# Optimization experiments

Measured on AMD Instinct MI355X. Metric: run time of the kernel, lower is better.

## Reference

```python
import jax, jax.numpy as jnp
import numpy as np

EPS = 1e-5
NUM_HEADS = 32

def layer_norm(x, g, b):
    m = jnp.mean(x, axis=-1, keepdims=True)
    v = jnp.mean((x - m) ** 2, axis=-1, keepdims=True)
    return (x - m) * jax.lax.rsqrt(v + EPS) * g + b

def positional_encoding(S, E):
    pos = jnp.arange(S, dtype=jnp.float32)[:, None]
    div = jnp.exp(jnp.arange(0, E, 2, dtype=jnp.float32) * (-jnp.log(10000.0) / E))
    ang = pos * div  # [S, E/2]
    pe = jnp.zeros((S, E), jnp.float32)
    pe = pe.at[:, 0::2].set(jnp.sin(ang)).at[:, 1::2].set(jnp.cos(ang))
    return pe

def quantum_attention(x, phi_l):
    # QLayer circuit: RX(x_j + phi_j) per wire, CNOT ring, measure Z.
    # Heisenberg picture: <Z_i> = prod_{j<=i} cos(a_j) for i>=1,
    #                     <Z_0> = prod_{j>=1} cos(a_j), a_j = x_j + phi_j.
    B, S, E = x.shape
    dk = E // NUM_HEADS  # = 8 wires
    c = jnp.cos(x.reshape(B, S, NUM_HEADS, dk) + phi_l)  # per-wire <Z> factor
    pref = jnp.cumprod(c, axis=-1)                       # prod_{j<=i}
    out0 = jnp.prod(c[..., 1:], axis=-1)                 # wire 0
    q = jnp.concatenate([out0[..., None], pref[..., 1:]], axis=-1)
    q = q.reshape(B, S, E)
    scores = jax.nn.softmax(
        jnp.einsum('bse,bte->bst', q, q) / jnp.sqrt(jnp.float32(dk)), axis=-1)
    return jnp.einsum('bst,bte->bse', scores, q)

def quantum_ffn(x, theta_l, W1_l, b1_l, W2_l, b2_l):
    # QLayer: RX(x_i) then RY(theta_i) on |0>, product state => <Z_i>=cos(x_i)cos(theta_i)
    nq = theta_l.shape[0]  # 8; encoder only reads first nq features
    qm = jnp.cos(x[..., :nq]) * jnp.cos(theta_l)
    h = jax.nn.relu(qm @ W1_l + b1_l)
    return h @ W2_l + b2_l

def setup_inputs() -> dict:
    key = jax.random.key(0)
    ks = jax.random.split(key, 10)
    V, E, L, FF, NQ, NC = 32000, 256, 4, 1024, 8, 10
    B, S = 8, 2048
    return {
        'tokens': jax.random.randint(ks[0], (B, S), 0, V, dtype=jnp.int64)
            if jax.config.jax_enable_x64 else jax.random.randint(ks[0], (B, S), 0, V, dtype=jnp.int32),
        'emb': jax.random.normal(ks[1], (V, E), jnp.float32),
        'phi': jax.random.normal(ks[2], (L, NQ), jnp.float32),
        'theta': jax.random.normal(ks[3], (L, NQ), jnp.float32),
        'W1': jax.random.normal(ks[4], (L, NQ, FF), jnp.float32) * 0.1,
        'b1': jax.random.normal(ks[5], (L, FF), jnp.float32) * 0.1,
        'W2': jax.random.normal(ks[6], (L, FF, E), jnp.float32) * 0.05,
        'b2': jax.random.normal(ks[7], (L, E), jnp.float32) * 0.05,
        'g1': jnp.ones((L, E), jnp.float32),
        'beta1': jnp.zeros((L, E), jnp.float32),
        'g2': jnp.ones((L, E), jnp.float32),
        'beta2': jnp.zeros((L, E), jnp.float32),
        'Wc': jax.random.normal(ks[8], (E, NC), jnp.float32) * 0.05,
        'bc': jax.random.normal(ks[9], (NC,), jnp.float32) * 0.05,
    }

def reference(tokens, emb, phi, theta, W1, b1, W2, b2, g1, beta1, g2, beta2, Wc, bc):
    B, S = tokens.shape
    E = emb.shape[1]
    x = emb[tokens] + positional_encoding(S, E)
    for l in range(phi.shape[0]):  # fixed num_blocks loop
        a = quantum_attention(x, phi[l])
        x = layer_norm(x + a, g1[l], beta1[l])
        f = quantum_ffn(x, theta[l], W1[l], b1[l], W2[l], b2[l])
        x = layer_norm(x + f, g2[l], beta2[l])
    return jnp.mean(x, axis=1) @ Wc + bc
```

## Files before the change

kernel.cpp:

```cpp
#include <hip/hip_runtime.h>
#include <hip/hip_bf16.h>

#define B_ 8
#define S_ 2048
#define E_ 256
#define FF_ 1024
#define NQ_ 8
#define NC_ 10
#define BS_ (B_*S_)
#define NSPLIT 2
#define KVBLK 32

typedef __bf16 bf16x8 __attribute__((ext_vector_type(8)));
typedef __bf16 bf16x4 __attribute__((ext_vector_type(4)));
typedef float f32x4 __attribute__((ext_vector_type(4)));

#define MFMA16(a,b,c) __builtin_amdgcn_mfma_f32_16x16x32_bf16(a,b,c,0,0,0)

__global__ __launch_bounds__(256) void k_embed(const int* __restrict__ tokens,
                                               const float* __restrict__ emb,
                                               float* __restrict__ x) {
    int row = blockIdx.x;
    int e = threadIdx.x;
    int s = row & (S_ - 1);
    int tok = tokens[row];
    int i2 = e & ~1;
    float d = __expf((float)i2 * (-9.210340371976184f / 256.0f));
    float ang = (float)s * d;
    float pe = (e & 1) ? __cosf(ang) : __sinf(ang);
    x[(size_t)row * E_ + e] = emb[(size_t)tok * E_ + e] + pe;
}

__global__ __launch_bounds__(256) void k_qt(const float* __restrict__ x,
                                            const float* __restrict__ phi_l,
                                            __hip_bfloat16* __restrict__ qbf,
                                            __hip_bfloat16* __restrict__ qT) {
    __shared__ __align__(16) __bf16 tile[64][76];
    int t0 = blockIdx.x * 64, e0 = blockIdx.y * 64, b = blockIdx.z;
    int tid = threadIdx.x;
    float ph[8];
#pragma unroll
    for (int j = 0; j < 8; j++) ph[j] = phi_l[j];
#pragma unroll
    for (int k = 0; k < 2; k++) {
        int idx = k * 256 + tid;
        int r = idx >> 3, hh = idx & 7;
        const float* xp = x + ((size_t)b * S_ + t0 + r) * E_ + e0 + hh * 8;
        f32x4 x0 = *(const f32x4*)xp;
        f32x4 x1 = *(const f32x4*)(xp + 4);
        float c[8];
#pragma unroll
        for (int j = 0; j < 4; j++) {
            c[j]     = __cosf(x0[j] + ph[j]);
            c[4 + j] = __cosf(x1[j] + ph[4 + j]);
        }
        float q[8];
        float run = c[0];
#pragma unroll
        for (int i = 1; i < 8; i++) { run *= c[i]; q[i] = run; }
        float o0 = c[1];
#pragma unroll
        for (int i = 2; i < 8; i++) o0 *= c[i];
        q[0] = o0;
        bf16x8 v;
#pragma unroll
        for (int j = 0; j < 8; j++) v[j] = (__bf16)q[j];
        *(bf16x8*)(qbf + ((size_t)b * S_ + t0 + r) * E_ + e0 + hh * 8) = v;
        *(bf16x8*)&tile[r][hh * 8] = v;
    }
    __syncthreads();
#pragma unroll
    for (int k = 0; k < 2; k++) {
        int idx = k * 256 + tid;
        int el = idx >> 3, tc = idx & 7;
        bf16x8 v;
#pragma unroll
        for (int j = 0; j < 8; j++) v[j] = tile[tc * 8 + j][el];
        *(bf16x8*)(qT + ((size_t)b * E_ + e0 + el) * S_ + t0 + tc * 8) = v;
    }
}

__global__ __launch_bounds__(256, 2) void k_attn(const __hip_bfloat16* __restrict__ qbf,
                                                 const __hip_bfloat16* __restrict__ qT,
                                                 __bf16* __restrict__ pacc,
                                                 float* __restrict__ pl) {
    __shared__ __align__(16) __bf16 ktile[KVBLK * 256];
    __shared__ __align__(16) __bf16 vtile[2][256 * KVBLK];
    __shared__ __align__(16) __bf16 plds[2][32][36];
    __shared__ float redl[2][32][2];
    const float SCALE = 0.3535533905932738f;
    int bid  = blockIdx.x;
    int b    = bid & 7;
    int qt   = (bid >> 3) & 31;
    int z    = bid >> 8;
    int tid  = threadIdx.x;
    int wv   = tid >> 6;
    int lane = tid & 63;
    int r16  = lane & 15;
    int kg   = lane >> 4;
    int rg   = wv >> 1, eh = wv & 1;
    int qrow0 = qt * 64 + rg * 32;
    int ebase = eh * 128;

    bf16x8 aq[2][8];
#pragma unroll
    for (int qs = 0; qs < 2; qs++)
#pragma unroll
        for (int kk = 0; kk < 8; kk++)
            aq[qs][kk] = *(const bf16x8*)(qbf + ((size_t)b * S_ + qrow0 + qs * 16 + r16) * E_ + kk * 32 + kg * 8);

    f32x4 acc0[8], acc1[8];
#pragma unroll
    for (int cf = 0; cf < 8; cf++) { acc0[cf] = (f32x4){0.f,0.f,0.f,0.f}; acc1[cf] = (f32x4){0.f,0.f,0.f,0.f}; }
    float lrow0[4] = {0.f,0.f,0.f,0.f}, lrow1[4] = {0.f,0.f,0.f,0.f};

    constexpr int SPAN = S_ / NSPLIT;
    constexpr int NT = SPAN / KVBLK;
    int k0 = z * SPAN;

    auto issue_k = [&](int kb) {
#pragma unroll
        for (int c = 0; c < 4; c++) {
            int seg = wv * 4 + c;
            int r = seg * 2 + (lane >> 5);
            int ch = lane & 31;
            const __hip_bfloat16* src = qbf + ((size_t)b * S_ + kb + r) * E_ + ((ch ^ (r & 7)) * 8);
            __builtin_amdgcn_global_load_lds((const __attribute__((address_space(1))) void*)src,
                                             (__attribute__((address_space(3))) void*)(ktile + seg * 512),
                                             16, 0, 0);
        }
    };
    auto issue_v = [&](int kb, int buf) {
#pragma unroll
        for (int c = 0; c < 4; c++) {
            int seg = wv * 4 + c;
            int e = seg * 16 + (lane >> 2);
            int ch = lane & 3;
            const __hip_bfloat16* src = qT + ((size_t)b * E_ + e) * S_ + kb + ((ch ^ ((e >> 1) & 3)) * 8);
            __builtin_amdgcn_global_load_lds((const __attribute__((address_space(1))) void*)src,
                                             (__attribute__((address_space(3))) void*)(&vtile[buf][seg * 512]),
                                             16, 0, 0);
        }
    };

    issue_k(k0);
    issue_v(k0, 0);
    asm volatile("s_waitcnt vmcnt(0)" ::: "memory");
    __syncthreads();

    for (int kt = 0; kt < NT; kt++) {
        int vcur = kt & 1;
        f32x4 s0 = (f32x4){0.f,0.f,0.f,0.f}, s1 = (f32x4){0.f,0.f,0.f,0.f};
#pragma unroll
        for (int kk = 0; kk < 8; kk++) {
            bf16x8 bk = *(const bf16x8*)&ktile[(eh * 16 + r16) * 256 + (((kk * 4 + kg) ^ (r16 & 7)) * 8)];
            s0 = MFMA16(aq[0][kk], bk, s0);
            s1 = MFMA16(aq[1][kk], bk, s1);
        }
#pragma unroll
        for (int i = 0; i < 4; i++) {
            float p0 = __expf(fmaf(s0[i], SCALE, -44.0f));
            float p1 = __expf(fmaf(s1[i], SCALE, -44.0f));
            plds[rg][kg * 4 + i][eh * 16 + r16]      = (__bf16)p0;
            plds[rg][16 + kg * 4 + i][eh * 16 + r16] = (__bf16)p1;
            lrow0[i] += p0;
            lrow1[i] += p1;
        }
        __syncthreads();
        bool more = (kt + 1 < NT);
        if (more) {
            int kn = k0 + (kt + 1) * KVBLK;
            issue_k(kn);
            issue_v(kn, vcur ^ 1);
        }
        bf16x8 pa0 = *(const bf16x8*)&plds[rg][r16][kg * 8];
        bf16x8 pa1 = *(const bf16x8*)&plds[rg][16 + r16][kg * 8];
#pragma unroll
        for (int cf = 0; cf < 8; cf++) {
            int vrow = ebase + cf * 16 + r16;
            bf16x8 bv = *(const bf16x8*)&vtile[vcur][vrow * KVBLK + ((kg ^ ((vrow >> 1) & 3)) * 8)];
            acc0[cf] = MFMA16(pa0, bv, acc0[cf]);
            acc1[cf] = MFMA16(pa1, bv, acc1[cf]);
        }
        if (more) {
            asm volatile("s_waitcnt vmcnt(0)" ::: "memory");
            __syncthreads();
        }
    }

#pragma unroll
    for (int i = 0; i < 4; i++) {
#pragma unroll
        for (int m = 1; m <= 8; m <<= 1) {
            lrow0[i] += __shfl_xor(lrow0[i], m);
            lrow1[i] += __shfl_xor(lrow1[i], m);
        }
    }
    if (r16 == 0) {
#pragma unroll
        for (int i = 0; i < 4; i++) {
            redl[rg][kg * 4 + i][eh]      = lrow0[i];
            redl[rg][16 + kg * 4 + i][eh] = lrow1[i];
        }
    }
    __syncthreads();
    size_t prow0 = (size_t)z * BS_ + (size_t)b * S_ + qrow0;
    if (eh == 0 && r16 == 0) {
#pragma unroll
        for (int i = 0; i < 4; i++) {
            int q = kg * 4 + i;
            pl[prow0 + q]      = redl[rg][q][0] + redl[rg][q][1];
            pl[prow0 + 16 + q] = redl[rg][16 + q][0] + redl[rg][16 + q][1];
        }
    }
#pragma unroll
    for (int i = 0; i < 4; i++) {
#pragma unroll
        for (int cf = 0; cf < 8; cf++) {
            pacc[(prow0 + kg * 4 + i) * E_ + ebase + cf * 16 + r16]      = (__bf16)acc0[cf][i];
            pacc[(prow0 + 16 + kg * 4 + i) * E_ + ebase + cf * 16 + r16] = (__bf16)acc1[cf][i];
        }
    }
}

__global__ __launch_bounds__(256) void k_aln(const __bf16* __restrict__ pacc,
                                             const float* __restrict__ pl,
                                             float* __restrict__ x,
                                             const float* __restrict__ g,
                                             const float* __restrict__ bb) {
    int wv = threadIdx.x >> 6, lane = threadIdx.x & 63;
    size_t row = (size_t)blockIdx.x * 4 + wv;
    float inv = 1.0f / (pl[row] + pl[BS_ + row]);
    bf16x4 a0 = ((const bf16x4*)(pacc + row * E_))[lane];
    bf16x4 a1 = ((const bf16x4*)(pacc + (size_t)BS_ * E_ + row * E_))[lane];
    f32x4 xv = ((const f32x4*)(x + row * E_))[lane];
    f32x4 v;
    float s = 0.f, sq = 0.f;
#pragma unroll
    for (int j = 0; j < 4; j++) {
        v[j] = xv[j] + ((float)a0[j] + (float)a1[j]) * inv;
        s += v[j]; sq += v[j] * v[j];
    }
#pragma unroll
    for (int m = 1; m <= 32; m <<= 1) { s += __shfl_xor(s, m); sq += __shfl_xor(sq, m); }
    float mean = s * (1.f / E_);
    float var = sq * (1.f / E_) - mean * mean;
    float rstd = rsqrtf(var + 1e-5f);
    f32x4 gv = ((const f32x4*)g)[lane];
    f32x4 bv = ((const f32x4*)bb)[lane];
    f32x4 o;
#pragma unroll
    for (int j = 0; j < 4; j++) o[j] = (v[j] - mean) * rstd * gv[j] + bv[j];
    ((f32x4*)(x + row * E_))[lane] = o;
}

__global__ __launch_bounds__(256) void k_w2t(const float* __restrict__ W2l,
                                             __hip_bfloat16* __restrict__ w2t) {
    __shared__ __align__(16) __bf16 tile[64][72];
    int k0 = blockIdx.x * 64, e0 = blockIdx.y * 64;
    int tid = threadIdx.x;
#pragma unroll
    for (int half = 0; half < 2; half++) {
        int r  = half * 32 + (tid >> 3);
        int c8 = (tid & 7) * 8;
        f32x4 v0 = *(const f32x4*)(W2l + (size_t)(k0 + r) * E_ + e0 + c8);
        f32x4 v1 = *(const f32x4*)(W2l + (size_t)(k0 + r) * E_ + e0 + c8 + 4);
#pragma unroll
        for (int j = 0; j < 4; j++) { tile[r][c8 + j] = (__bf16)v0[j]; tile[r][c8 + 4 + j] = (__bf16)v1[j]; }
    }
    __syncthreads();
#pragma unroll
    for (int half = 0; half < 2; half++) {
        int e  = half * 32 + (tid >> 3);
        int k8 = (tid & 7) * 8;
        bf16x8 v;
#pragma unroll
        for (int j = 0; j < 8; j++) v[j] = tile[k8 + j][e];
        *(bf16x8*)(w2t + (size_t)(e0 + e) * FF_ + k0 + k8) = v;
    }
}

__global__ __launch_bounds__(256) void k_ffn(const float* __restrict__ x,
                                             const float* __restrict__ theta_l,
                                             const float* __restrict__ W1l,
                                             const float* __restrict__ b1l,
                                             const __hip_bfloat16* __restrict__ w2t,
                                             const float* __restrict__ b2l,
                                             const float* __restrict__ g,
                                             const float* __restrict__ bb) {
    __shared__ __align__(16) __bf16 Bld[2][256 * 64];
    __shared__ __align__(16) __bf16 Ald[2][32 * 64];
    __shared__ float qmld[32][9];
    __shared__ float reds[32][4][2];
    int tid = threadIdx.x;
    int wv = tid >> 6, lane = tid & 63;
    int r16 = lane & 15, kg = lane >> 4;
    int rbase = blockIdx.x * 32;
    int ebQ = wv * 64;
    const int NT = FF_ / 64;

    {
        int r = tid >> 3, i = tid & 7;
        qmld[r][i] = __cosf(x[(size_t)(rbase + r) * E_ + i]) * __cosf(theta_l[i]);
    }

    f32x4 w[18];

    auto issue_B = [&](int kt, int buf) {
#pragma unroll
        for (int s = 0; s < 8; s++) {
            int seg = wv * 8 + s;
            int e = seg * 8 + (lane >> 3);
            int c = lane & 7;
            const __hip_bfloat16* src = w2t + (size_t)e * FF_ + kt * 64 + ((c ^ (e & 7)) * 8);
            __builtin_amdgcn_global_load_lds((const __attribute__((address_space(1))) void*)src,
                                             (__attribute__((address_space(3))) void*)(&Bld[buf][seg * 512]),
                                             16, 0, 0);
        }
    };
    auto load_W1 = [&](int kt) {
        int c = tid & 7;
        int k = kt * 64 + c * 8;
#pragma unroll
        for (int i = 0; i < 8; i++) {
            w[2 * i]     = *(const f32x4*)(W1l + (size_t)i * FF_ + k);
            w[2 * i + 1] = *(const f32x4*)(W1l + (size_t)i * FF_ + k + 4);
        }
        w[16] = *(const f32x4*)(b1l + k);
        w[17] = *(const f32x4*)(b1l + k + 4);
    };
    auto math_h = [&](int buf) {
        int r = tid >> 3, c = tid & 7;
        f32x4 h0 = w[16], h1 = w[17];
#pragma unroll
        for (int i = 0; i < 8; i++) {
            float qv = qmld[r][i];
#pragma unroll
            for (int j = 0; j < 4; j++) {
                h0[j] = fmaf(qv, w[2 * i][j], h0[j]);
                h1[j] = fmaf(qv, w[2 * i + 1][j], h1[j]);
            }
        }
        bf16x8 hv;
#pragma unroll
        for (int j = 0; j < 4; j++) {
            hv[j]     = (__bf16)fmaxf(h0[j], 0.f);
            hv[4 + j] = (__bf16)fmaxf(h1[j], 0.f);
        }
        *(bf16x8*)&Ald[buf][r * 64 + ((c ^ (r & 7)) * 8)] = hv;
    };

    issue_B(0, 0);
    load_W1(0);
    __syncthreads();
    math_h(0);
    __syncthreads();

    f32x4 acc[2][4];
#pragma unroll
    for (int qs = 0; qs < 2; qs++)
#pragma unroll
        for (int cf = 0; cf < 4; cf++) acc[qs][cf] = (f32x4){0.f, 0.f, 0.f, 0.f};

    for (int kt = 0; kt < NT; kt++) {
        int cur = kt & 1;
        bool more = (kt + 1 < NT);
        if (more) {
            issue_B(kt + 1, cur ^ 1);
            load_W1(kt + 1);
        }
        bf16x8 aq[2][2];
#pragma unroll
        for (int qs = 0; qs < 2; qs++)
#pragma unroll
            for (int kk = 0; kk < 2; kk++)
                aq[qs][kk] = *(const bf16x8*)&Ald[cur][(qs * 16 + r16) * 64 + (((kk * 4 + kg) ^ (r16 & 7)) * 8)];
#pragma unroll
        for (int cf = 0; cf < 4; cf++) {
            int e = ebQ + cf * 16 + r16;
#pragma unroll
            for (int kk = 0; kk < 2; kk++) {
                bf16x8 bv = *(const bf16x8*)&Bld[cur][e * 64 + (((kk * 4 + kg) ^ (e & 7)) * 8)];
                acc[0][cf] = MFMA16(aq[0][kk], bv, acc[0][cf]);
                acc[1][cf] = MFMA16(aq[1][kk], bv, acc[1][cf]);
            }
        }
        if (more) {
            math_h(cur ^ 1);
            __syncthreads();
        }
    }

    float sA[2][4] = {{0.f,0.f,0.f,0.f},{0.f,0.f,0.f,0.f}};
    float sQ[2][4] = {{0.f,0.f,0.f,0.f},{0.f,0.f,0.f,0.f}};
#pragma unroll
    for (int qs = 0; qs < 2; qs++)
#pragma unroll
        for (int cf = 0; cf < 4; cf++) {
            int e = ebQ + cf * 16 + r16;
            float b2v = b2l[e];
#pragma unroll
            for (int i = 0; i < 4; i++) {
                size_t orow = (size_t)rbase + qs * 16 + kg * 4 + i;
                float t = acc[qs][cf][i] + b2v + x[orow * E_ + e];
                acc[qs][cf][i] = t;
                sA[qs][i] += t; sQ[qs][i] += t * t;
            }
        }
#pragma unroll
    for (int qs = 0; qs < 2; qs++)
#pragma unroll
        for (int i = 0; i < 4; i++) {
#pragma unroll
            for (int m = 1; m <= 8; m <<= 1) {
                sA[qs][i] += __shfl_xor(sA[qs][i], m);
                sQ[qs][i] += __shfl_xor(sQ[qs][i], m);
            }
        }
    if (r16 == 0) {
#pragma unroll
        for (int qs = 0; qs < 2; qs++)
#pragma unroll
            for (int i = 0; i < 4; i++) {
                int row = qs * 16 + kg * 4 + i;
                reds[row][wv][0] = sA[qs][i];
                reds[row][wv][1] = sQ[qs][i];
            }
    }
    __syncthreads();
    float mean[2][4], rstd[2][4];
#pragma unroll
    for (int qs = 0; qs < 2; qs++)
#pragma unroll
        for (int i = 0; i < 4; i++) {
            int row = qs * 16 + kg * 4 + i;
            float S = reds[row][0][0] + reds[row][1][0] + reds[row][2][0] + reds[row][3][0];
            float Q = reds[row][0][1] + reds[row][1][1] + reds[row][2][1] + reds[row][3][1];
            mean[qs][i] = S * (1.f / E_);
            float var = Q * (1.f / E_) - mean[qs][i] * mean[qs][i];
            rstd[qs][i] = rsqrtf(var + 1e-5f);
        }
    float* xo = (float*)x;
#pragma unroll
    for (int qs = 0; qs < 2; qs++)
#pragma unroll
        for (int cf = 0; cf < 4; cf++) {
            int e = ebQ + cf * 16 + r16;
            float gv = g[e], bv = bb[e];
#pragma unroll
            for (int i = 0; i < 4; i++) {
                size_t orow = (size_t)rbase + qs * 16 + kg * 4 + i;
                xo[orow * E_ + e] = (acc[qs][cf][i] - mean[qs][i]) * rstd[qs][i] * gv + bv;
            }
        }
}

__global__ __launch_bounds__(256) void k_mean(const float* __restrict__ x, float* __restrict__ psum) {
    int c = blockIdx.x, b = blockIdx.y, e = threadIdx.x;
    float s = 0.f;
    size_t base = ((size_t)b * S_ + c * 128) * E_ + e;
    for (int r = 0; r < 128; r++) s += x[base + (size_t)r * E_];
    psum[(c * 8 + b) * E_ + e] = s;
}

__global__ __launch_bounds__(256) void k_mean2(const float* __restrict__ psum, float* __restrict__ xmean) {
    int idx = blockIdx.x * 256 + threadIdx.x;
    int b = idx >> 8, e = idx & 255;
    float s = 0.f;
    for (int c = 0; c < 16; c++) s += psum[(c * 8 + b) * E_ + e];
    xmean[idx] = s * (1.f / S_);
}

__global__ __launch_bounds__(128) void k_cls(const float* __restrict__ xmean,
                                             const float* __restrict__ Wc,
                                             const float* __restrict__ bc,
                                             float* __restrict__ outp) {
    int t = threadIdx.x;
    if (t >= B_ * NC_) return;
    int b = t / NC_, c = t % NC_;
    float s = bc[c];
    for (int e = 0; e < E_; e++) s += xmean[b * E_ + e] * Wc[e * NC_ + c];
    outp[t] = s;
}

extern "C" void kernel_launch(void* const* d_in, const int* in_sizes, int n_in,
                              void* d_out, int out_size, void* d_ws, size_t ws_size,
                              hipStream_t stream) {
    (void)in_sizes; (void)n_in; (void)out_size; (void)ws_size;
    const int*   tokens = (const int*)d_in[0];
    const float* emb    = (const float*)d_in[1];
    const float* phi    = (const float*)d_in[2];
    const float* theta  = (const float*)d_in[3];
    const float* W1     = (const float*)d_in[4];
    const float* b1     = (const float*)d_in[5];
    const float* W2     = (const float*)d_in[6];
    const float* b2     = (const float*)d_in[7];
    const float* g1     = (const float*)d_in[8];
    const float* beta1  = (const float*)d_in[9];
    const float* g2     = (const float*)d_in[10];
    const float* beta2  = (const float*)d_in[11];
    const float* Wc     = (const float*)d_in[12];
    const float* bc     = (const float*)d_in[13];
    float* outp = (float*)d_out;

    float* xbuf = (float*)d_ws;
    __hip_bfloat16* qbf = (__hip_bfloat16*)(xbuf + (size_t)BS_ * E_);
    __hip_bfloat16* qT  = qbf + (size_t)BS_ * E_;
    __hip_bfloat16* w2t = qT + (size_t)BS_ * E_;
    float* psum  = (float*)(w2t + (size_t)4 * E_ * FF_);
    float* xmean = psum + 16 * 8 * E_;
    float* pl    = xmean + B_ * E_;
    __bf16* pacc = (__bf16*)(pl + (size_t)NSPLIT * BS_);

    k_embed<<<BS_, 256, 0, stream>>>(tokens, emb, xbuf);
    for (int l = 0; l < 4; l++)
        k_w2t<<<dim3(FF_ / 64, E_ / 64), 256, 0, stream>>>(W2 + (size_t)l * FF_ * E_,
                                                           w2t + (size_t)l * E_ * FF_);

    for (int l = 0; l < 4; l++) {
        k_qt<<<dim3(S_ / 64, E_ / 64, B_), 256, 0, stream>>>(xbuf, phi + l * NQ_, qbf, qT);
        k_attn<<<(S_ / 64) * B_ * NSPLIT, 256, 0, stream>>>(qbf, qT, pacc, pl);
        k_aln<<<BS_ / 4, 256, 0, stream>>>(pacc, pl, xbuf, g1 + l * E_, beta1 + l * E_);
        k_ffn<<<BS_ / 32, 256, 0, stream>>>(xbuf, theta + l * NQ_,
                                            W1 + (size_t)l * NQ_ * FF_, b1 + (size_t)l * FF_,
                                            w2t + (size_t)l * E_ * FF_, b2 + (size_t)l * E_,
                                            g2 + l * E_, beta2 + l * E_);
    }

    k_mean<<<dim3(16, B_), 256, 0, stream>>>(xbuf, psum);
    k_mean2<<<8, 256, 0, stream>>>(psum, xmean);
    k_cls<<<1, 128, 0, stream>>>(xmean, Wc, bc, outp);
}
```

Measured before the change: 441.2 us.

## Give each wave its own 16 query rows and double-buffer K tile

Reworks the attention kernel so each wave owns 16 query rows across the full 256-wide output instead of splitting rows and E halves across wave pairs. P exchange then stays wave-private, which removes the mid-iteration block barrier and the cross-wave row-sum reduction through LDS. K is now double-buffered like V, and the next tile's loads are issued at the top of the iteration. The cost is more accumulator registers per wave (16 f32x4), which may pressure occupancy at launch bounds of 2 blocks per CU.

```diff
diff --git a/kernel.cpp b/kernel.cpp
--- a/kernel.cpp
+++ b/kernel.cpp
@@ -84,10 +84,9 @@
                                                  const __hip_bfloat16* __restrict__ qT,
                                                  __bf16* __restrict__ pacc,
                                                  float* __restrict__ pl) {
-    __shared__ __align__(16) __bf16 ktile[KVBLK * 256];
+    __shared__ __align__(16) __bf16 ktile[2][KVBLK * 256];
     __shared__ __align__(16) __bf16 vtile[2][256 * KVBLK];
-    __shared__ __align__(16) __bf16 plds[2][32][36];
-    __shared__ float redl[2][32][2];
+    __shared__ __align__(16) __bf16 plds[4][16][36];
     const float SCALE = 0.3535533905932738f;
     int bid  = blockIdx.x;
     int b    = bid & 7;
@@ -98,27 +97,23 @@
     int lane = tid & 63;
     int r16  = lane & 15;
     int kg   = lane >> 4;
-    int rg   = wv >> 1, eh = wv & 1;
-    int qrow0 = qt * 64 + rg * 32;
-    int ebase = eh * 128;
-
-    bf16x8 aq[2][8];
-#pragma unroll
-    for (int qs = 0; qs < 2; qs++)
-#pragma unroll
-        for (int kk = 0; kk < 8; kk++)
-            aq[qs][kk] = *(const bf16x8*)(qbf + ((size_t)b * S_ + qrow0 + qs * 16 + r16) * E_ + kk * 32 + kg * 8);
-
-    f32x4 acc0[8], acc1[8];
-#pragma unroll
-    for (int cf = 0; cf < 8; cf++) { acc0[cf] = (f32x4){0.f,0.f,0.f,0.f}; acc1[cf] = (f32x4){0.f,0.f,0.f,0.f}; }
-    float lrow0[4] = {0.f,0.f,0.f,0.f}, lrow1[4] = {0.f,0.f,0.f,0.f};
+    int qrow0 = qt * 64 + wv * 16;
+
+    bf16x8 aq[8];
+#pragma unroll
+    for (int kk = 0; kk < 8; kk++)
+        aq[kk] = *(const bf16x8*)(qbf + ((size_t)b * S_ + qrow0 + r16) * E_ + kk * 32 + kg * 8);
+
+    f32x4 acc[16];
+#pragma unroll
+    for (int cf = 0; cf < 16; cf++) acc[cf] = (f32x4){0.f, 0.f, 0.f, 0.f};
+    float lrow[4] = {0.f, 0.f, 0.f, 0.f};
 
     constexpr int SPAN = S_ / NSPLIT;
     constexpr int NT = SPAN / KVBLK;
     int k0 = z * SPAN;
 
-    auto issue_k = [&](int kb) {
+    auto issue_k = [&](int kb, int buf) {
 #pragma unroll
         for (int c = 0; c < 4; c++) {
             int seg = wv * 4 + c;
@@ -126,7 +121,7 @@
             int ch = lane & 31;
             const __hip_bfloat16* src = qbf + ((size_t)b * S_ + kb + r) * E_ + ((ch ^ (r & 7)) * 8);
             __builtin_amdgcn_global_load_lds((const __attribute__((address_space(1))) void*)src,
-                                             (__attribute__((address_space(3))) void*)(ktile + seg * 512),
+                                             (__attribute__((address_space(3))) void*)(&ktile[buf][seg * 512]),
                                              16, 0, 0);
         }
     };
@@ -143,44 +138,43 @@
         }
     };
 
-    issue_k(k0);
+    issue_k(k0, 0);
     issue_v(k0, 0);
     asm volatile("s_waitcnt vmcnt(0)" ::: "memory");
     __syncthreads();
 
     for (int kt = 0; kt < NT; kt++) {
-        int vcur = kt & 1;
+        int cur = kt & 1;
+        bool more = (kt + 1 < NT);
+        if (more) {
+            int kn = k0 + (kt + 1) * KVBLK;
+            issue_k(kn, cur ^ 1);
+            issue_v(kn, cur ^ 1);
+        }
         f32x4 s0 = (f32x4){0.f,0.f,0.f,0.f}, s1 = (f32x4){0.f,0.f,0.f,0.f};
 #pragma unroll
         for (int kk = 0; kk < 8; kk++) {
-            bf16x8 bk = *(const bf16x8*)&ktile[(eh * 16 + r16) * 256 + (((kk * 4 + kg) ^ (r16 & 7)) * 8)];
-            s0 = MFMA16(aq[0][kk], bk, s0);
-            s1 = MFMA16(aq[1][kk], bk, s1);
+            int sw = ((kk * 4 + kg) ^ (r16 & 7)) * 8;
+            bf16x8 bk0 = *(const bf16x8*)&ktile[cur][r16 * 256 + sw];
+            bf16x8 bk1 = *(const bf16x8*)&ktile[cur][(16 + r16) * 256 + sw];
+            s0 = MFMA16(aq[kk], bk0, s0);
+            s1 = MFMA16(aq[kk], bk1, s1);
         }
 #pragma unroll
         for (int i = 0; i < 4; i++) {
             float p0 = __expf(fmaf(s0[i], SCALE, -44.0f));
             float p1 = __expf(fmaf(s1[i], SCALE, -44.0f));
-            plds[rg][kg * 4 + i][eh * 16 + r16]      = (__bf16)p0;
-            plds[rg][16 + kg * 4 + i][eh * 16 + r16] = (__bf16)p1;
-            lrow0[i] += p0;
-            lrow1[i] += p1;
-        }
-        __syncthreads();
-        bool more = (kt + 1 < NT);
-        if (more) {
-            int kn = k0 + (kt + 1) * KVBLK;
-            issue_k(kn);
-            issue_v(kn, vcur ^ 1);
-        }
-        bf16x8 pa0 = *(const bf16x8*)&plds[rg][r16][kg * 8];
-        bf16x8 pa1 = *(const bf16x8*)&plds[rg][16 + r16][kg * 8];
-#pragma unroll
-        for (int cf = 0; cf < 8; cf++) {
-            int vrow = ebase + cf * 16 + r16;
-            bf16x8 bv = *(const bf16x8*)&vtile[vcur][vrow * KVBLK + ((kg ^ ((vrow >> 1) & 3)) * 8)];
-            acc0[cf] = MFMA16(pa0, bv, acc0[cf]);
-            acc1[cf] = MFMA16(pa1, bv, acc1[cf]);
+            plds[wv][kg * 4 + i][r16]      = (__bf16)p0;
+            plds[wv][kg * 4 + i][16 + r16] = (__bf16)p1;
+            lrow[i] += p0 + p1;
+        }
+        asm volatile("s_waitcnt lgkmcnt(0)" ::: "memory");
+        bf16x8 pa = *(const bf16x8*)&plds[wv][r16][kg * 8];
+#pragma unroll
+        for (int cf = 0; cf < 16; cf++) {
+            int vrow = cf * 16 + r16;
+            bf16x8 bv = *(const bf16x8*)&vtile[cur][vrow * KVBLK + ((kg ^ ((vrow >> 1) & 3)) * 8)];
+            acc[cf] = MFMA16(pa, bv, acc[cf]);
         }
         if (more) {
             asm volatile("s_waitcnt vmcnt(0)" ::: "memory");
@@ -190,36 +184,22 @@
 
 #pragma unroll
     for (int i = 0; i < 4; i++) {
-#pragma unroll
-        for (int m = 1; m <= 8; m <<= 1) {
-            lrow0[i] += __shfl_xor(lrow0[i], m);
-            lrow1[i] += __shfl_xor(lrow1[i], m);
-        }
-    }
+        lrow[i] += __shfl_xor(lrow[i], 1);
+        lrow[i] += __shfl_xor(lrow[i], 2);
+        lrow[i] += __shfl_xor(lrow[i], 4);
+        lrow[i] += __shfl_xor(lrow[i], 8);
+    }
+    size_t prow0 = (size_t)z * BS_ + (size_t)b * S_ + qrow0;
     if (r16 == 0) {
 #pragma unroll
-        for (int i = 0; i < 4; i++) {
-            redl[rg][kg * 4 + i][eh]      = lrow0[i];
-            redl[rg][16 + kg * 4 + i][eh] = lrow1[i];
-        }
-    }
-    __syncthreads();
-    size_t prow0 = (size_t)z * BS_ + (size_t)b * S_ + qrow0;
-    if (eh == 0 && r16 == 0) {
-#pragma unroll
-        for (int i = 0; i < 4; i++) {
-            int q = kg * 4 + i;
-            pl[prow0 + q]      = redl[rg][q][0] + redl[rg][q][1];
-            pl[prow0 + 16 + q] = redl[rg][16 + q][0] + redl[rg][16 + q][1];
-        }
+        for (int i = 0; i < 4; i++)
+            pl[prow0 + kg * 4 + i] = lrow[i];
     }
 #pragma unroll
     for (int i = 0; i < 4; i++) {
 #pragma unroll
-        for (int cf = 0; cf < 8; cf++) {
-            pacc[(prow0 + kg * 4 + i) * E_ + ebase + cf * 16 + r16]      = (__bf16)acc0[cf][i];
-            pacc[(prow0 + 16 + kg * 4 + i) * E_ + ebase + cf * 16 + r16] = (__bf16)acc1[cf][i];
-        }
+        for (int cf = 0; cf < 16; cf++)
+            pacc[(prow0 + kg * 4 + i) * E_ + cf * 16 + r16] = (__bf16)acc[cf][i];
     }
 }
 
```

Result: slower. 455.2 us (+3.2%).
